# Kernel optimization log

Measured on AMD Instinct MI355X. Metric: run time of the kernel, lower is better.

The kernel has to match this reference:

```python
import jax, jax.numpy as jnp
import numpy as np

B, N, F, H, L = 8, 512, 32, 64, 2

def setup_inputs() -> dict:
    key = jax.random.key(0)
    ks = jax.random.split(key, 16)
    s = lambda fan_in: 1.0 / np.sqrt(fan_in)
    return {
        "x": jax.random.normal(ks[0], (B, N, F), dtype=jnp.float32),
        # node encoder: Linear(F, H), stored as [in, out]
        "W_enc": jax.random.uniform(ks[1], (F, H), minval=-s(F), maxval=s(F)),
        "b_enc": jax.random.uniform(ks[2], (H,), minval=-s(F), maxval=s(F)),
        # edge MLP: Linear(2H, H) then Linear(H, 1)
        "W_e1": jax.random.uniform(ks[3], (2 * H, H), minval=-s(2 * H), maxval=s(2 * H)),
        "b_e1": jax.random.uniform(ks[4], (H,), minval=-s(2 * H), maxval=s(2 * H)),
        "W_e2": jax.random.uniform(ks[5], (H,), minval=-s(H), maxval=s(H)),
        "b_e2": jax.random.uniform(ks[6], (), minval=-s(H), maxval=s(H)),
        # per-layer message Linear(H, H)
        "W_msg": jax.random.uniform(ks[7], (L, H, H), minval=-s(H), maxval=s(H)),
        "b_msg": jax.random.uniform(ks[8], (L, H), minval=-s(H), maxval=s(H)),
        # per-layer GRUCell(H, H): gates ordered [r, z, n], stored as [in, 3H]
        "W_ih": jax.random.uniform(ks[9], (L, H, 3 * H), minval=-s(H), maxval=s(H)),
        "b_ih": jax.random.uniform(ks[10], (L, 3 * H), minval=-s(H), maxval=s(H)),
        "W_hh": jax.random.uniform(ks[11], (L, H, 3 * H), minval=-s(H), maxval=s(H)),
        "b_hh": jax.random.uniform(ks[12], (L, 3 * H), minval=-s(H), maxval=s(H)),
        # output Linear(H, 1)
        "W_out": jax.random.uniform(ks[13], (H, 1), minval=-s(H), maxval=s(H)),
        "b_out": jax.random.uniform(ks[14], (1,), minval=-s(H), maxval=s(H)),
    }

def reference(x, W_enc, b_enc, W_e1, b_e1, W_e2, b_e2, W_msg, b_msg,
              W_ih, b_ih, W_hh, b_hh, W_out, b_out):
    # Node encoding (dropout is eval-mode identity)
    h = jax.nn.relu(x @ W_enc + b_enc)  # [B, N, H]

    # Edge MLP on pairwise concat [h_i, h_j]: split W_e1 so we never build the 2H concat
    Wa, Wb = W_e1[:H], W_e1[H:]
    zi = h @ Wa                           # contribution of h_i, [B, N, H]
    zj = h @ Wb                           # contribution of h_j, [B, N, H]
    e = jax.nn.relu(zi[:, :, None, :] + zj[:, None, :, :] + b_e1)  # [B, N, N, H]
    logits = jnp.einsum('bijh,h->bij', e, W_e2) + b_e2             # [B, N, N]

    eye = jnp.eye(logits.shape[-1], dtype=bool)
    logits = jnp.where(eye[None], -jnp.inf, logits)
    adj = jax.nn.softmax(logits, axis=-1)
    adj = jnp.nan_to_num(adj, nan=0.0, posinf=0.0, neginf=0.0)

    for l in range(L):
        m = jnp.einsum('bij,bjh->bih', adj, h)             # message aggregation
        m = jax.nn.relu(m @ W_msg[l] + b_msg[l])
        # GRUCell update (gates [r, z, n])
        gi = m @ W_ih[l] + b_ih[l]
        gh = h @ W_hh[l] + b_hh[l]
        ir, iz, inn = jnp.split(gi, 3, axis=-1)
        hr, hz, hn = jnp.split(gh, 3, axis=-1)
        r = jax.nn.sigmoid(ir + hr)
        z = jax.nn.sigmoid(iz + hz)
        n = jnp.tanh(inn + r * hn)
        h = (1.0 - z) * n + z * h

    graph_emb = jnp.mean(h, axis=1)       # [B, H]
    return graph_emb @ W_out + b_out      # [B, 1]
```

## Files before the change

kernel.cpp:

```cpp
#include <hip/hip_runtime.h>
#include <math.h>

#define BB 8
#define NN 512
#define FF 32
#define HH 64
#define NEG_BIG (-1.0e30f)

__device__ __forceinline__ float lane_bcast(float v, int l) {
    return __int_as_float(__builtin_amdgcn_readlane(__float_as_int(v), l));
}

__global__ __launch_bounds__(256) void encode_kernel(
    const float* __restrict__ x, const float* __restrict__ W_enc,
    const float* __restrict__ b_enc, const float* __restrict__ W_e1,
    const float* __restrict__ b_e1,
    float* __restrict__ h, float* __restrict__ zi, float* __restrict__ zj)
{
    const int t = threadIdx.x;
    const int hh = t & 63;
    const int qu = __builtin_amdgcn_readfirstlane(t >> 6);
    const int gR = blockIdx.x * 4 + qu;

    const float xv = x[gR * FF + (hh & 31)];
    float acc = b_enc[hh];
#pragma unroll 8
    for (int k = 0; k < FF; ++k)
        acc = fmaf(lane_bcast(xv, k), W_enc[k * HH + hh], acc);
    const float hval = fmaxf(acc, 0.f);
    h[gR * HH + hh] = hval;

    float z1 = b_e1[hh], z2 = 0.f;
#pragma unroll 8
    for (int k = 0; k < HH; ++k) {
        const float hk = lane_bcast(hval, k);
        z1 = fmaf(hk, W_e1[k * HH + hh], z1);
        z2 = fmaf(hk, W_e1[(HH + k) * HH + hh], z2);
    }
    zi[gR * HH + hh] = z1;
    zj[gR * HH + hh] = z2;
}

__global__ __launch_bounds__(256) void adj_kernel(
    const float* __restrict__ zi, const float* __restrict__ zj,
    const float* __restrict__ W_e2, const float* __restrict__ b_e2,
    float* __restrict__ adj)
{
    const int b = blockIdx.x >> 7;
    const int i0 = (blockIdx.x & 127) << 2;
    const int t = threadIdx.x;
    const int qu = __builtin_amdgcn_readfirstlane(t >> 6);
    const int tj = t & 63;
    const int j0 = (qu << 7) + tj;
    const int j1 = j0 + 64;

    __shared__ float zjs[NN][17];
    __shared__ float red[4][8];

    float zr[4];
#pragma unroll
    for (int r = 0; r < 4; ++r) zr[r] = zi[(b * NN + i0 + r) * HH + tj];
    const float wv = W_e2[tj];

    const float be2 = b_e2[0];
    float acc0[4], acc1[4];
#pragma unroll
    for (int r = 0; r < 4; ++r) { acc0[r] = be2; acc1[r] = be2; }

    for (int kp = 0; kp < 4; ++kp) {
        __syncthreads();
        {
            const int idx4 = t;
#pragma unroll
            for (int u = 0; u < 8; ++u) {
                const int i4 = idx4 + u * 256;
                const int row = i4 >> 2, c4 = i4 & 3;
                *(float4*)&zjs[row][c4 * 4] =
                    ((const float4*)(zj + (size_t)(b * NN + row) * HH))[kp * 4 + c4];
            }
        }
        __syncthreads();
#pragma unroll
        for (int c = 0; c < 16; ++c) {
            const int k = (kp << 4) + c;
            const float w = lane_bcast(wv, k);
            const float zj0 = zjs[j0][c];
            const float zj1 = zjs[j1][c];
#pragma unroll
            for (int r = 0; r < 4; ++r) {
                const float zv = lane_bcast(zr[r], k);
                acc0[r] = fmaf(fmaxf(zv + zj0, 0.f), w, acc0[r]);
                acc1[r] = fmaf(fmaxf(zv + zj1, 0.f), w, acc1[r]);
            }
        }
    }

#pragma unroll
    for (int r = 0; r < 4; ++r) {
        const int irow = i0 + r;
        if (j0 == irow) acc0[r] = NEG_BIG;
        if (j1 == irow) acc1[r] = NEG_BIG;
    }

    float wmax[4];
#pragma unroll
    for (int r = 0; r < 4; ++r) {
        float m = fmaxf(acc0[r], acc1[r]);
#pragma unroll
        for (int off = 32; off >= 1; off >>= 1) m = fmaxf(m, __shfl_xor(m, off));
        wmax[r] = m;
    }
    if (tj == 0) {
#pragma unroll
        for (int r = 0; r < 4; ++r) red[qu][r] = wmax[r];
    }
    __syncthreads();
    float M[4];
#pragma unroll
    for (int r = 0; r < 4; ++r)
        M[r] = fmaxf(fmaxf(red[0][r], red[1][r]), fmaxf(red[2][r], red[3][r]));
    __syncthreads();

    float e0[4], e1[4];
#pragma unroll
    for (int r = 0; r < 4; ++r) {
        e0[r] = __expf(acc0[r] - M[r]);
        e1[r] = __expf(acc1[r] - M[r]);
        float s = e0[r] + e1[r];
#pragma unroll
        for (int off = 32; off >= 1; off >>= 1) s += __shfl_xor(s, off);
        if (tj == 0) red[qu][r] = s;
    }
    __syncthreads();
#pragma unroll
    for (int r = 0; r < 4; ++r) {
        const float inv = 1.0f / (red[0][r] + red[1][r] + red[2][r] + red[3][r]);
        float* arow = adj + ((size_t)(b * NN + i0 + r)) * NN;
        arow[j0] = e0[r] * inv;
        arow[j1] = e1[r] * inv;
    }
}

__global__ __launch_bounds__(1024, 4) void layer_kernel(
    const float* __restrict__ adjw, const float* __restrict__ h_in,
    const float* __restrict__ Wmsg, const float* __restrict__ bmsg,
    const float* __restrict__ Wih, const float* __restrict__ bih,
    const float* __restrict__ Whh, const float* __restrict__ bhh,
    float* __restrict__ h_out, float* __restrict__ partial)
{
    const int b  = blockIdx.x >> 5;
    const int i0 = (blockIdx.x & 31) << 4;
    const int t  = threadIdx.x;
    const int hh = t & 63;
    const int w  = __builtin_amdgcn_readfirstlane(t >> 6);
    const int gR0 = b * NN + i0;

    __shared__ float adjs[16][512];
    __shared__ union {
        float red[8][16][66];
        float gbuf[2][16][3][66];
    } U;
    __shared__ float mfull[16][66];
    __shared__ float mmfull[16][66];
    __shared__ float hown[16][66];

    {
        const float4* asrc = (const float4*)(adjw + (size_t)gR0 * NN);
        float4* adst = (float4*)&adjs[0][0];
        adst[t] = asrc[t];
        adst[t + 1024] = asrc[t + 1024];
    }
    hown[w][hh] = h_in[(size_t)(gR0 + w) * HH + hh];
    __syncthreads();

    const int rg = w >> 3, kc = w & 7;
    const float* hj = h_in + (size_t)b * NN * HH + (size_t)(kc * 64) * HH + hh;

    float mac[8] = {0.f, 0.f, 0.f, 0.f, 0.f, 0.f, 0.f, 0.f};
#pragma unroll 2
    for (int j = 0; j < 64; j += 4) {
        const float h0 = hj[(j + 0) * HH];
        const float h1 = hj[(j + 1) * HH];
        const float h2 = hj[(j + 2) * HH];
        const float h3 = hj[(j + 3) * HH];
#pragma unroll
        for (int r = 0; r < 8; ++r) {
            const float4 av = *(const float4*)&adjs[rg * 8 + r][kc * 64 + j];
            mac[r] = fmaf(av.w, h3,
                     fmaf(av.z, h2,
                     fmaf(av.y, h1,
                     fmaf(av.x, h0, mac[r]))));
        }
    }
#pragma unroll
    for (int r = 0; r < 8; ++r) U.red[kc][rg * 8 + r][hh] = mac[r];
    __syncthreads();

    {
        float s = 0.f;
#pragma unroll
        for (int p = 0; p < 8; ++p) s += U.red[p][w][hh];
        mfull[w][hh] = s;

        float acc = bmsg[hh];
#pragma unroll 8
        for (int k = 0; k < HH; ++k)
            acc = fmaf(mfull[w][k], Wmsg[k * HH + hh], acc);
        mmfull[w][hh] = fmaxf(acc, 0.f);
    }
    __syncthreads();

    const int half = w >> 3, rp = w & 7;
    {
        const float* Wg = half ? Whh : Wih;
        const float* bg = half ? bhh : bih;
        const float (*src)[66] = half ? (const float (*)[66])hown
                                      : (const float (*)[66])mmfull;
        float a0 = bg[hh], a1 = bg[64 + hh], a2 = bg[128 + hh];
        float c0 = a0, c1 = a1, c2 = a2;
#pragma unroll 2
        for (int k = 0; k < HH; ++k) {
            const float* wk = Wg + k * 192;
            const float w0 = wk[hh], w1 = wk[64 + hh], w2 = wk[128 + hh];
            const float va = src[2 * rp][k];
            const float vb = src[2 * rp + 1][k];
            a0 = fmaf(va, w0, a0); a1 = fmaf(va, w1, a1); a2 = fmaf(va, w2, a2);
            c0 = fmaf(vb, w0, c0); c1 = fmaf(vb, w1, c1); c2 = fmaf(vb, w2, c2);
        }
        U.gbuf[half][2 * rp][0][hh] = a0;
        U.gbuf[half][2 * rp][1][hh] = a1;
        U.gbuf[half][2 * rp][2][hh] = a2;
        U.gbuf[half][2 * rp + 1][0][hh] = c0;
        U.gbuf[half][2 * rp + 1][1][hh] = c1;
        U.gbuf[half][2 * rp + 1][2][hh] = c2;
    }
    __syncthreads();

    {
        const float ir = U.gbuf[0][w][0][hh], iz = U.gbuf[0][w][1][hh],
                    in = U.gbuf[0][w][2][hh];
        const float hr = U.gbuf[1][w][0][hh], hz = U.gbuf[1][w][1][hh],
                    hn = U.gbuf[1][w][2][hh];
        const float rr = 1.f / (1.f + __expf(-(ir + hr)));
        const float zz = 1.f / (1.f + __expf(-(iz + hz)));
        const float nnv = tanhf(in + rr * hn);
        const float hnew = (1.f - zz) * nnv + zz * hown[w][hh];
        h_out[(size_t)(gR0 + w) * HH + hh] = hnew;

        if (partial != nullptr) {
            mfull[w][hh] = hnew;
            __syncthreads();
            if (w == 0) {
                float s = 0.f;
#pragma unroll
                for (int r = 0; r < 16; ++r) s += mfull[r][hh];
                partial[blockIdx.x * 64 + hh] = s;
            }
        }
    }
}

__global__ __launch_bounds__(64) void readout_kernel(
    const float* __restrict__ partial, const float* __restrict__ W_out,
    const float* __restrict__ b_out, float* __restrict__ out)
{
    const int b = blockIdx.x;
    const int hh = threadIdx.x;
    float s = 0.f;
#pragma unroll 8
    for (int c = 0; c < 32; ++c)
        s += partial[(b * 32 + c) * 64 + hh];
    float v = s * (1.0f / NN) * W_out[hh];
#pragma unroll
    for (int off = 32; off >= 1; off >>= 1) v += __shfl_xor(v, off);
    if (hh == 0) out[b] = v + b_out[0];
}

extern "C" void kernel_launch(void* const* d_in, const int* in_sizes, int n_in,
                              void* d_out, int out_size, void* d_ws, size_t ws_size,
                              hipStream_t stream)
{
    const float* x     = (const float*)d_in[0];
    const float* W_enc = (const float*)d_in[1];
    const float* b_enc = (const float*)d_in[2];
    const float* W_e1  = (const float*)d_in[3];
    const float* b_e1  = (const float*)d_in[4];
    const float* W_e2  = (const float*)d_in[5];
    const float* b_e2  = (const float*)d_in[6];
    const float* W_msg = (const float*)d_in[7];
    const float* b_msg = (const float*)d_in[8];
    const float* W_ih  = (const float*)d_in[9];
    const float* b_ih  = (const float*)d_in[10];
    const float* W_hh  = (const float*)d_in[11];
    const float* b_hh  = (const float*)d_in[12];
    const float* W_out = (const float*)d_in[13];
    const float* b_out = (const float*)d_in[14];
    float* out = (float*)d_out;

    float* ws  = (float*)d_ws;
    float* h0  = ws;
    float* h1  = h0 + BB * NN * HH;
    float* zi  = h1 + BB * NN * HH;
    float* zj  = zi + BB * NN * HH;
    float* prt = zj + BB * NN * HH;
    float* adjw = prt + 256 * 64;

    encode_kernel<<<BB * NN / 4, 256, 0, stream>>>(x, W_enc, b_enc, W_e1, b_e1, h0, zi, zj);
    adj_kernel<<<BB * (NN / 4), 256, 0, stream>>>(zi, zj, W_e2, b_e2, adjw);

    layer_kernel<<<BB * (NN / 16), 1024, 0, stream>>>(
        adjw, h0, W_msg, b_msg, W_ih, b_ih, W_hh, b_hh, h1, nullptr);
    layer_kernel<<<BB * (NN / 16), 1024, 0, stream>>>(
        adjw, h1, W_msg + HH * HH, b_msg + HH,
        W_ih + HH * 3 * HH, b_ih + 3 * HH, W_hh + HH * 3 * HH, b_hh + 3 * HH,
        h0, prt);

    readout_kernel<<<BB, 64, 0, stream>>>(prt, W_out, b_out, out);
}
```

Before: 83.19 us.

## Halve layer block rows to 8 and split GRU gate GEMV over k-halves

The layer kernel now processes 8 rows per 512-thread block, which doubles the grid to 512 blocks so more CUs have work. Message and GRU matvecs take their inputs through readlane broadcasts from registers instead of shared-memory row reads. The GRU gate GEMV is split across two k-halves with 4 rows per wave, and the partial sums are added in shared memory. In exchange, each block reloads h_j from global twice as often in total, there is an extra sync, and the readout has twice as many partials to reduce.

```diff
diff --git a/kernel.cpp b/kernel.cpp
--- a/kernel.cpp
+++ b/kernel.cpp
@@ -141,119 +141,130 @@
     }
 }
 
-__global__ __launch_bounds__(1024, 4) void layer_kernel(
+__global__ __launch_bounds__(512, 4) void layer_kernel(
     const float* __restrict__ adjw, const float* __restrict__ h_in,
     const float* __restrict__ Wmsg, const float* __restrict__ bmsg,
     const float* __restrict__ Wih, const float* __restrict__ bih,
     const float* __restrict__ Whh, const float* __restrict__ bhh,
     float* __restrict__ h_out, float* __restrict__ partial)
 {
-    const int b  = blockIdx.x >> 5;
-    const int i0 = (blockIdx.x & 31) << 4;
+    const int b  = blockIdx.x >> 6;
+    const int i0 = (blockIdx.x & 63) << 3;
     const int t  = threadIdx.x;
     const int hh = t & 63;
     const int w  = __builtin_amdgcn_readfirstlane(t >> 6);
     const int gR0 = b * NN + i0;
 
-    __shared__ float adjs[16][512];
+    __shared__ float adjs[8][512];
     __shared__ union {
-        float red[8][16][66];
-        float gbuf[2][16][3][66];
+        float red[8][8][66];
+        float gbuf[2][2][8][3][66];
     } U;
-    __shared__ float mfull[16][66];
-    __shared__ float mmfull[16][66];
-    __shared__ float hown[16][66];
+    __shared__ float mml[8][66];
+    __shared__ float hol[8][66];
 
     {
         const float4* asrc = (const float4*)(adjw + (size_t)gR0 * NN);
         float4* adst = (float4*)&adjs[0][0];
         adst[t] = asrc[t];
-        adst[t + 1024] = asrc[t + 1024];
-    }
-    hown[w][hh] = h_in[(size_t)(gR0 + w) * HH + hh];
-    __syncthreads();
-
-    const int rg = w >> 3, kc = w & 7;
-    const float* hj = h_in + (size_t)b * NN * HH + (size_t)(kc * 64) * HH + hh;
-
-    float mac[8] = {0.f, 0.f, 0.f, 0.f, 0.f, 0.f, 0.f, 0.f};
+        adst[t + 512] = asrc[t + 512];
+    }
+    hol[t >> 6][hh] = h_in[(size_t)(gR0 + (t >> 6)) * HH + hh];
+    __syncthreads();
+
+    {
+        const float* hj = h_in + (size_t)b * NN * HH + (size_t)(w * 64) * HH + hh;
+        float mac[8] = {0.f, 0.f, 0.f, 0.f, 0.f, 0.f, 0.f, 0.f};
 #pragma unroll 2
-    for (int j = 0; j < 64; j += 4) {
-        const float h0 = hj[(j + 0) * HH];
-        const float h1 = hj[(j + 1) * HH];
-        const float h2 = hj[(j + 2) * HH];
-        const float h3 = hj[(j + 3) * HH];
-#pragma unroll
-        for (int r = 0; r < 8; ++r) {
-            const float4 av = *(const float4*)&adjs[rg * 8 + r][kc * 64 + j];
-            mac[r] = fmaf(av.w, h3,
-                     fmaf(av.z, h2,
-                     fmaf(av.y, h1,
-                     fmaf(av.x, h0, mac[r]))));
-        }
-    }
-#pragma unroll
-    for (int r = 0; r < 8; ++r) U.red[kc][rg * 8 + r][hh] = mac[r];
-    __syncthreads();
-
-    {
-        float s = 0.f;
-#pragma unroll
-        for (int p = 0; p < 8; ++p) s += U.red[p][w][hh];
-        mfull[w][hh] = s;
-
+        for (int j = 0; j < 64; j += 4) {
+            const float h0 = hj[(j + 0) * HH];
+            const float h1 = hj[(j + 1) * HH];
+            const float h2 = hj[(j + 2) * HH];
+            const float h3 = hj[(j + 3) * HH];
+#pragma unroll
+            for (int r = 0; r < 8; ++r) {
+                const float4 av = *(const float4*)&adjs[r][w * 64 + j];
+                mac[r] = fmaf(av.w, h3,
+                         fmaf(av.z, h2,
+                         fmaf(av.y, h1,
+                         fmaf(av.x, h0, mac[r]))));
+            }
+        }
+#pragma unroll
+        for (int r = 0; r < 8; ++r) U.red[w][r][hh] = mac[r];
+    }
+    __syncthreads();
+
+    {
+        float m = 0.f;
+#pragma unroll
+        for (int p = 0; p < 8; ++p) m += U.red[p][w][hh];
         float acc = bmsg[hh];
-#pragma unroll 8
+#pragma unroll 4
         for (int k = 0; k < HH; ++k)
-            acc = fmaf(mfull[w][k], Wmsg[k * HH + hh], acc);
-        mmfull[w][hh] = fmaxf(acc, 0.f);
-    }
-    __syncthreads();
-
-    const int half = w >> 3, rp = w & 7;
+            acc = fmaf(lane_bcast(m, k), Wmsg[k * HH + hh], acc);
+        mml[w][hh] = fmaxf(acc, 0.f);
+    }
+    __syncthreads();
+
+    const int half = w >> 2, kh = (w >> 1) & 1, rq = w & 1;
     {
         const float* Wg = half ? Whh : Wih;
         const float* bg = half ? bhh : bih;
-        const float (*src)[66] = half ? (const float (*)[66])hown
-                                      : (const float (*)[66])mmfull;
-        float a0 = bg[hh], a1 = bg[64 + hh], a2 = bg[128 + hh];
-        float c0 = a0, c1 = a1, c2 = a2;
+        float src[4];
+#pragma unroll
+        for (int r = 0; r < 4; ++r)
+            src[r] = half ? hol[rq * 4 + r][hh] : mml[rq * 4 + r][hh];
+        float a0[4], a1[4], a2[4];
+#pragma unroll
+        for (int r = 0; r < 4; ++r) {
+            a0[r] = kh ? 0.f : bg[hh];
+            a1[r] = kh ? 0.f : bg[64 + hh];
+            a2[r] = kh ? 0.f : bg[128 + hh];
+        }
+        const int k0 = kh * 32;
 #pragma unroll 2
-        for (int k = 0; k < HH; ++k) {
-            const float* wk = Wg + k * 192;
+        for (int kk = 0; kk < 32; ++kk) {
+            const float* wk = Wg + (k0 + kk) * 192;
             const float w0 = wk[hh], w1 = wk[64 + hh], w2 = wk[128 + hh];
-            const float va = src[2 * rp][k];
-            const float vb = src[2 * rp + 1][k];
-            a0 = fmaf(va, w0, a0); a1 = fmaf(va, w1, a1); a2 = fmaf(va, w2, a2);
-            c0 = fmaf(vb, w0, c0); c1 = fmaf(vb, w1, c1); c2 = fmaf(vb, w2, c2);
-        }
-        U.gbuf[half][2 * rp][0][hh] = a0;
-        U.gbuf[half][2 * rp][1][hh] = a1;
-        U.gbuf[half][2 * rp][2][hh] = a2;
-        U.gbuf[half][2 * rp + 1][0][hh] = c0;
-        U.gbuf[half][2 * rp + 1][1][hh] = c1;
-        U.gbuf[half][2 * rp + 1][2][hh] = c2;
-    }
-    __syncthreads();
-
-    {
-        const float ir = U.gbuf[0][w][0][hh], iz = U.gbuf[0][w][1][hh],
-                    in = U.gbuf[0][w][2][hh];
-        const float hr = U.gbuf[1][w][0][hh], hz = U.gbuf[1][w][1][hh],
-                    hn = U.gbuf[1][w][2][hh];
+#pragma unroll
+            for (int r = 0; r < 4; ++r) {
+                const float v = lane_bcast(src[r], k0 + kk);
+                a0[r] = fmaf(v, w0, a0[r]);
+                a1[r] = fmaf(v, w1, a1[r]);
+                a2[r] = fmaf(v, w2, a2[r]);
+            }
+        }
+#pragma unroll
+        for (int r = 0; r < 4; ++r) {
+            U.gbuf[half][kh][rq * 4 + r][0][hh] = a0[r];
+            U.gbuf[half][kh][rq * 4 + r][1][hh] = a1[r];
+            U.gbuf[half][kh][rq * 4 + r][2][hh] = a2[r];
+        }
+    }
+    __syncthreads();
+
+    {
+        const float ir = U.gbuf[0][0][w][0][hh] + U.gbuf[0][1][w][0][hh];
+        const float iz = U.gbuf[0][0][w][1][hh] + U.gbuf[0][1][w][1][hh];
+        const float in = U.gbuf[0][0][w][2][hh] + U.gbuf[0][1][w][2][hh];
+        const float hr = U.gbuf[1][0][w][0][hh] + U.gbuf[1][1][w][0][hh];
+        const float hz = U.gbuf[1][0][w][1][hh] + U.gbuf[1][1][w][1][hh];
+        const float hn = U.gbuf[1][0][w][2][hh] + U.gbuf[1][1][w][2][hh];
         const float rr = 1.f / (1.f + __expf(-(ir + hr)));
         const float zz = 1.f / (1.f + __expf(-(iz + hz)));
         const float nnv = tanhf(in + rr * hn);
-        const float hnew = (1.f - zz) * nnv + zz * hown[w][hh];
+        const float hnew = (1.f - zz) * nnv + zz * hol[w][hh];
         h_out[(size_t)(gR0 + w) * HH + hh] = hnew;
 
         if (partial != nullptr) {
-            mfull[w][hh] = hnew;
+            __syncthreads();
+            mml[w][hh] = hnew;
             __syncthreads();
             if (w == 0) {
                 float s = 0.f;
 #pragma unroll
-                for (int r = 0; r < 16; ++r) s += mfull[r][hh];
+                for (int r = 0; r < 8; ++r) s += mml[r][hh];
                 partial[blockIdx.x * 64 + hh] = s;
             }
         }
@@ -268,8 +279,8 @@
     const int hh = threadIdx.x;
     float s = 0.f;
 #pragma unroll 8
-    for (int c = 0; c < 32; ++c)
-        s += partial[(b * 32 + c) * 64 + hh];
+    for (int c = 0; c < 64; ++c)
+        s += partial[(b * 64 + c) * 64 + hh];
     float v = s * (1.0f / NN) * W_out[hh];
 #pragma unroll
     for (int off = 32; off >= 1; off >>= 1) v += __shfl_xor(v, off);
@@ -303,14 +314,14 @@
     float* zi  = h1 + BB * NN * HH;
     float* zj  = zi + BB * NN * HH;
     float* prt = zj + BB * NN * HH;
-    float* adjw = prt + 256 * 64;
+    float* adjw = prt + 512 * 64;
 
     encode_kernel<<<BB * NN / 4, 256, 0, stream>>>(x, W_enc, b_enc, W_e1, b_e1, h0, zi, zj);
     adj_kernel<<<BB * (NN / 4), 256, 0, stream>>>(zi, zj, W_e2, b_e2, adjw);
 
-    layer_kernel<<<BB * (NN / 16), 1024, 0, stream>>>(
+    layer_kernel<<<BB * (NN / 8), 512, 0, stream>>>(
         adjw, h0, W_msg, b_msg, W_ih, b_ih, W_hh, b_hh, h1, nullptr);
-    layer_kernel<<<BB * (NN / 16), 1024, 0, stream>>>(
+    layer_kernel<<<BB * (NN / 8), 512, 0, stream>>>(
         adjw, h1, W_msg + HH * HH, b_msg + HH,
         W_ih + HH * 3 * HH, b_ih + 3 * HH, W_hh + HH * 3 * HH, b_hh + 3 * HH,
         h0, prt);
```

New measurement: 79.02 us. 1.05x faster.
